# Kernel tuning notes

Hardware: AMD Instinct MI355X
Metric: run time of the kernel (lower is better)

The kernel has to match this reference:

```python
import jax, jax.numpy as jnp
import numpy as np

N, F, H, K = 4096, 512, 256, 8
NEG = -1e9


def _attention(h, mask, a_w, a_b):
    # h: [N,H]; mask: [N,N] bool; a_w: [K,2H]; a_b: [K]
    # per-head logits[i,j] = lrelu(a_src . h_i + a_dst . h_j + b), softmax over
    # neighbors j (A[i,j]==1); out_i = h_i + sum_j alpha_ij h_j; isolated nodes
    # (no neighbors) keep h_i unchanged (alpha row masked to zero).
    Hd = h.shape[1]
    src = h @ a_w[:, :Hd].T + a_b[None, :]   # [N,K]
    dst = h @ a_w[:, Hd:].T                  # [N,K]
    fmask = mask.astype(h.dtype)
    outs = []
    for k in range(a_w.shape[0]):
        logits = jax.nn.leaky_relu(src[:, k][:, None] + dst[:, k][None, :], 0.01)
        logits = jnp.where(mask, logits, NEG)
        alpha = jax.nn.softmax(logits, axis=1) * fmask  # zero rows for isolated nodes
        outs.append(h + alpha @ h)
    return outs


def setup_inputs() -> dict:
    key = jax.random.key(0)
    ks = jax.random.split(key, 12)
    s = 0.02
    adjacency = jax.random.randint(ks[0], (N, N), 0, 2).astype(jnp.float32)
    feats = jax.random.normal(ks[1], (N, F), dtype=jnp.float32)
    return {
        "adjacency": adjacency,
        "feats": feats,
        "W1_w": jax.random.normal(ks[2], (H, F), dtype=jnp.float32) * s,
        "W1_b": jnp.zeros((H,), jnp.float32),
        "a1_w": jax.random.normal(ks[3], (K, 2 * H), dtype=jnp.float32) * s,
        "a1_b": jnp.zeros((K,), jnp.float32),
        "W2_w": jax.random.normal(ks[4], (H, K * H), dtype=jnp.float32) * s,
        "W2_b": jnp.zeros((H,), jnp.float32),
        "a2_w": jax.random.normal(ks[5], (K, 2 * H), dtype=jnp.float32) * s,
        "a2_b": jnp.zeros((K,), jnp.float32),
        "out_w": jax.random.normal(ks[6], (1, H), dtype=jnp.float32) * s,
        "out_b": jnp.zeros((1,), jnp.float32),
    }


def reference(adjacency, feats, W1_w, W1_b, a1_w, a1_b, W2_w, W2_b, a2_w, a2_b, out_w, out_b):
    mask = adjacency == 1.0
    # torch.inner(A, feats.T) == A @ feats; dropout is identity in eval mode
    h1 = (adjacency @ feats) @ W1_w.T + W1_b            # [N,H]
    heads1 = _attention(h1, mask, a1_w, a1_b)           # K x [N,H]
    h1_new = jax.nn.elu(jnp.concatenate(heads1, axis=1))  # [N,K*H]
    h2 = h1_new @ W2_w.T + W2_b                         # [N,H]
    heads2 = _attention(h2, mask, a2_w, a2_b)
    avg = sum(heads2) / a2_w.shape[0]                   # [N,H]
    h2_new = jax.nn.elu(avg)
    avgd = jnp.mean(h2_new, axis=0)                     # [H]
    return avgd @ out_w.T + out_b                       # [1]
```

## Files before the change

### kernel.cpp

```cpp
#include <hip/hip_runtime.h>
#include <hip/hip_bf16.h>
#include <hip/hip_fp16.h>


#define NN 4096
#define FF 512
#define HH 256
#define KK 8
#define KH 2048

typedef __attribute__((ext_vector_type(8))) short bf16x8;
typedef __attribute__((ext_vector_type(4))) float f32x4;
typedef __attribute__((ext_vector_type(16))) float f32x16;
typedef _Float16 h16x2 __attribute__((ext_vector_type(2)));
typedef _Float16 h16x8 __attribute__((ext_vector_type(8)));

__device__ inline short f2bf(float x) {
    __hip_bfloat16 b = __float2bfloat16(x);
    return *reinterpret_cast<short*>(&b);
}
__device__ inline short to_bf(float x) { return f2bf(x); }
__device__ inline short to_bf(short x) { return x; }

__device__ inline unsigned int pkh(float a, float b) {
    auto r = __builtin_amdgcn_cvt_pkrtz(a, b);
    unsigned int u;
    __builtin_memcpy(&u, &r, 4);
    return u;
}
__device__ inline unsigned int h2mul(unsigned int a, unsigned int b) {
    h16x2 av, bv;
    __builtin_memcpy(&av, &a, 4);
    __builtin_memcpy(&bv, &b, 4);
    h16x2 r = av * bv;
    unsigned int u;
    __builtin_memcpy(&u, &r, 4);
    return u;
}
__device__ inline unsigned int h2max(unsigned int a, unsigned int b) {
    h16x2 av, bv;
    __builtin_memcpy(&av, &a, 4);
    __builtin_memcpy(&bv, &b, 4);
    h16x2 r = __builtin_elementwise_max(av, bv);
    unsigned int u;
    __builtin_memcpy(&u, &r, 4);
    return u;
}
__device__ inline float h2dot1(unsigned int a, float c) {
    h16x2 av;
    __builtin_memcpy(&av, &a, 4);
    h16x2 one = {(_Float16)1.0f, (_Float16)1.0f};
    return __builtin_amdgcn_fdot2(av, one, c, false);
}

__device__ inline unsigned int enc_f(float x) {
    unsigned int u = __float_as_uint(x);
    return (u & 0x80000000u) ? ~u : (u | 0x80000000u);
}
__device__ inline float dec_f(unsigned int e) {
    unsigned int u = (e & 0x80000000u) ? (e ^ 0x80000000u) : ~e;
    return __uint_as_float(u);
}

__global__ void pack_mask_kernel(const float* __restrict__ adj,
                                 unsigned int* __restrict__ mbits) {
    int i = blockIdx.x;
    int lane = threadIdx.x & 63;
    int wv = threadIdx.x >> 6;
    for (int j0 = wv * 64; j0 < NN; j0 += 256) {
        float v = adj[(size_t)i * NN + j0 + lane];
        unsigned long long b = __ballot(v == 1.0f);
        if (lane == 0) {
            mbits[i * 128 + (j0 >> 5)]     = (unsigned int)(b & 0xffffffffull);
            mbits[i * 128 + (j0 >> 5) + 1] = (unsigned int)(b >> 32);
        }
    }
}

template <typename T>
__global__ __launch_bounds__(256) void cvt_a_frag_kernel(const T* __restrict__ src,
                                                         bf16x8* __restrict__ dst, int K) {
    int t = threadIdx.x, lane = t & 63, w = t >> 6, mt = blockIdx.x;
    int Kt = K >> 5;
    int m = mt * 16 + (lane & 15), kq = (lane >> 4) * 8;
    for (int kt = w; kt < Kt; kt += 4) {
        size_t base = (size_t)m * K + kt * 32 + kq;
        bf16x8 v;
#pragma unroll
        for (int jj = 0; jj < 8; jj++) v[jj] = to_bf(src[base + jj]);
        dst[((size_t)mt * Kt + kt) * 64 + lane] = v;
    }
}

__global__ __launch_bounds__(256) void cvt_bt_frag_kernel(const float* __restrict__ Wm,
                                                          bf16x8* __restrict__ dst,
                                                          int K, int Nt) {
    int t = threadIdx.x, lane = t & 63, w = t >> 6, nt = blockIdx.x;
    int Kt = K >> 5;
    int n = nt * 16 + (lane & 15), kq = (lane >> 4) * 8;
    for (int kt = w; kt < Kt; kt += 4) {
        size_t base = (size_t)n * K + kt * 32 + kq;
        bf16x8 v;
#pragma unroll
        for (int jj = 0; jj < 8; jj++) v[jj] = f2bf(Wm[base + jj]);
        dst[((size_t)kt * Nt + nt) * 64 + lane] = v;
    }
}

template <int W>
__global__ __launch_bounds__(256) void cvt_b_frag_kernel(const float* __restrict__ src,
                                                         bf16x8* __restrict__ dst) {
    __shared__ float hs[32][W + 8];
    constexpr int Nt = W / 16;
    int t = threadIdx.x, jb = blockIdx.x;
    {
        int r = t >> 3, cb = (t & 7) * (W / 8);
        const float* sp = &src[(size_t)(jb * 32 + r) * W + cb];
#pragma unroll
        for (int q = 0; q < W / 32; q++) *(float4*)&hs[r][cb + q * 4] = *(const float4*)&sp[q * 4];
    }
    __syncthreads();
    for (int id = t; id < Nt * 64; id += 256) {
        int nt = id >> 6, lane = id & 63;
        int c = nt * 16 + (lane & 15), q8 = (lane >> 4) * 8;
        bf16x8 v;
#pragma unroll
        for (int jj = 0; jj < 8; jj++) v[jj] = f2bf(hs[q8 + jj][c]);
        dst[((size_t)jb * Nt + nt) * 64 + lane] = v;
    }
}

__global__ __launch_bounds__(256) void gemm_frag_kernel(
    const bf16x8* __restrict__ Af, const bf16x8* __restrict__ Bf,
    const float* __restrict__ bias, float* __restrict__ C,
    int Kt, int Nt, int Nrow) {
    int t = threadIdx.x, lane = t & 63, w = t >> 6;
    int quad = lane >> 4, c16 = lane & 15;
    int wm = w & 1, wn = w >> 1;
    int mt0 = blockIdx.y * 4 + wm * 2;
    int nt0 = blockIdx.x * 8 + wn * 4;
    f32x4 acc[2][4];
#pragma unroll
    for (int i = 0; i < 2; i++)
#pragma unroll
        for (int j = 0; j < 4; j++) acc[i][j] = (f32x4){0.f, 0.f, 0.f, 0.f};
    const bf16x8* ap = Af + (size_t)mt0 * Kt * 64 + lane;
    const bf16x8* bp = Bf + (size_t)nt0 * 64 + lane;
#pragma unroll 2
    for (int kt = 0; kt < Kt; kt++) {
        bf16x8 a0 = ap[(size_t)kt * 64];
        bf16x8 a1 = ap[((size_t)Kt + kt) * 64];
        bf16x8 b0 = bp[(size_t)kt * Nt * 64];
        bf16x8 b1 = bp[((size_t)kt * Nt + 1) * 64];
        bf16x8 b2 = bp[((size_t)kt * Nt + 2) * 64];
        bf16x8 b3 = bp[((size_t)kt * Nt + 3) * 64];
        acc[0][0] = __builtin_amdgcn_mfma_f32_16x16x32_bf16(a0, b0, acc[0][0], 0, 0, 0);
        acc[0][1] = __builtin_amdgcn_mfma_f32_16x16x32_bf16(a0, b1, acc[0][1], 0, 0, 0);
        acc[0][2] = __builtin_amdgcn_mfma_f32_16x16x32_bf16(a0, b2, acc[0][2], 0, 0, 0);
        acc[0][3] = __builtin_amdgcn_mfma_f32_16x16x32_bf16(a0, b3, acc[0][3], 0, 0, 0);
        acc[1][0] = __builtin_amdgcn_mfma_f32_16x16x32_bf16(a1, b0, acc[1][0], 0, 0, 0);
        acc[1][1] = __builtin_amdgcn_mfma_f32_16x16x32_bf16(a1, b1, acc[1][1], 0, 0, 0);
        acc[1][2] = __builtin_amdgcn_mfma_f32_16x16x32_bf16(a1, b2, acc[1][2], 0, 0, 0);
        acc[1][3] = __builtin_amdgcn_mfma_f32_16x16x32_bf16(a1, b3, acc[1][3], 0, 0, 0);
    }
#pragma unroll
    for (int i = 0; i < 2; i++) {
#pragma unroll
        for (int j = 0; j < 4; j++) {
            int n = (nt0 + j) * 16 + c16;
            float bv = bias ? bias[n] : 0.f;
#pragma unroll
            for (int reg = 0; reg < 4; reg++) {
                int m = (mt0 + i) * 16 + quad * 4 + reg;
                C[(size_t)m * Nrow + n] = acc[i][j][reg] + bv;
            }
        }
    }
}

__global__ __launch_bounds__(256) void gemm_adj_kernel(
    const unsigned int* __restrict__ mbits, const bf16x8* __restrict__ Bf,
    float* __restrict__ C, int Kt, int Nt, int Nrow) {
    int t = threadIdx.x, lane = t & 63, w = t >> 6;
    int quad = lane >> 4, c16 = lane & 15;
    int wm = w & 1, wn = w >> 1;
    int mt0 = blockIdx.y * 4 + wm * 2;
    int nt0 = blockIdx.x * 8 + wn * 4;
    int m = lane & 15, q8 = (lane >> 4) * 8;
    int row0 = mt0 * 16 + m, row1 = row0 + 16;
    f32x4 acc[2][4];
#pragma unroll
    for (int i = 0; i < 2; i++)
#pragma unroll
        for (int j = 0; j < 4; j++) acc[i][j] = (f32x4){0.f, 0.f, 0.f, 0.f};
    const bf16x8* bp = Bf + (size_t)nt0 * 64 + lane;
#pragma unroll 2
    for (int kt = 0; kt < Kt; kt++) {
        unsigned int w0 = mbits[(size_t)row0 * 128 + kt];
        unsigned int w1 = mbits[(size_t)row1 * 128 + kt];
        unsigned int mb0 = (w0 >> q8) & 0xffu;
        unsigned int mb1 = (w1 >> q8) & 0xffu;
        union { unsigned int u[4]; bf16x8 v; } A0, A1;
#pragma unroll
        for (int jp = 0; jp < 4; jp++) {
            unsigned int u0 = (mb0 >> (2 * jp)) & 3u;
            unsigned int u1 = (mb1 >> (2 * jp)) & 3u;
            A0.u[jp] = ((u0 * 0x8001u) & 0x10001u) * 0x3F80u;
            A1.u[jp] = ((u1 * 0x8001u) & 0x10001u) * 0x3F80u;
        }
        bf16x8 b0 = bp[(size_t)kt * Nt * 64];
        bf16x8 b1 = bp[((size_t)kt * Nt + 1) * 64];
        bf16x8 b2 = bp[((size_t)kt * Nt + 2) * 64];
        bf16x8 b3 = bp[((size_t)kt * Nt + 3) * 64];
        acc[0][0] = __builtin_amdgcn_mfma_f32_16x16x32_bf16(A0.v, b0, acc[0][0], 0, 0, 0);
        acc[0][1] = __builtin_amdgcn_mfma_f32_16x16x32_bf16(A0.v, b1, acc[0][1], 0, 0, 0);
        acc[0][2] = __builtin_amdgcn_mfma_f32_16x16x32_bf16(A0.v, b2, acc[0][2], 0, 0, 0);
        acc[0][3] = __builtin_amdgcn_mfma_f32_16x16x32_bf16(A0.v, b3, acc[0][3], 0, 0, 0);
        acc[1][0] = __builtin_amdgcn_mfma_f32_16x16x32_bf16(A1.v, b0, acc[1][0], 0, 0, 0);
        acc[1][1] = __builtin_amdgcn_mfma_f32_16x16x32_bf16(A1.v, b1, acc[1][1], 0, 0, 0);
        acc[1][2] = __builtin_amdgcn_mfma_f32_16x16x32_bf16(A1.v, b2, acc[1][2], 0, 0, 0);
        acc[1][3] = __builtin_amdgcn_mfma_f32_16x16x32_bf16(A1.v, b3, acc[1][3], 0, 0, 0);
    }
#pragma unroll
    for (int i = 0; i < 2; i++) {
#pragma unroll
        for (int j = 0; j < 4; j++) {
            int n = (nt0 + j) * 16 + c16;
#pragma unroll
            for (int reg = 0; reg < 4; reg++) {
                int mm = (mt0 + i) * 16 + quad * 4 + reg;
                C[(size_t)mm * Nrow + n] = acc[i][j][reg];
            }
        }
    }
}

__global__ __launch_bounds__(256) void prep_kernel(const float* __restrict__ h,
                                                   const float* __restrict__ aw,
                                                   const float* __restrict__ ab,
                                                   h16x8* __restrict__ HB16,
                                                   float* __restrict__ srcT,
                                                   float* __restrict__ dstT,
                                                   unsigned int* __restrict__ maxd_u) {
    __shared__ __align__(16) float hs[32][264];
    __shared__ __align__(16) float awl[KK * 512];
    int t = threadIdx.x, jb = blockIdx.x;
#pragma unroll
    for (int q = 0; q < 4; q++)
        *(float4*)&awl[(t + q * 256) * 4] = *(const float4*)&aw[(t + q * 256) * 4];
    {
        int r = t >> 3, cb = (t & 7) * 32;
        const float* hp = &h[(size_t)(jb * 32 + r) * HH + cb];
#pragma unroll
        for (int q = 0; q < 8; q++) *(float4*)&hs[r][cb + q * 4] = *(const float4*)&hp[q * 4];
    }
    __syncthreads();
#pragma unroll
    for (int it = 0; it < 4; it++) {
        int id = t + it * 256;
        int q = id >> 9, nt = (id >> 6) & 7, lane = id & 63;
        int c = nt * 32 + (lane & 31), j8 = q * 16 + (lane >> 5) * 8;
        union { unsigned int u[4]; h16x8 v; } pk;
#pragma unroll
        for (int jp = 0; jp < 4; jp++)
            pk.u[jp] = pkh(hs[j8 + 2 * jp][c], hs[j8 + 2 * jp + 1][c]);
        HB16[((size_t)(jb * 2 + q)) * 512 + nt * 64 + lane] = pk.v;
    }
    {
        const float LOG2E = 1.4426950408889634f;
        int row = t & 31, head = t >> 5;
        float s = ab[head], d = 0.f;
        const float* ws = &awl[head * 512];
        const float* wd = ws + 256;
#pragma unroll 4
        for (int c = 0; c < 256; c += 4) {
            float4 hv = *(const float4*)&hs[row][c];
            float4 a4 = *(const float4*)&ws[c];
            float4 b4 = *(const float4*)&wd[c];
            s += hv.x * a4.x + hv.y * a4.y + hv.z * a4.z + hv.w * a4.w;
            d += hv.x * b4.x + hv.y * b4.y + hv.z * b4.z + hv.w * b4.w;
        }
        float ds = d * LOG2E;
        srcT[head * NN + jb * 32 + row] = s * LOG2E;
        dstT[head * NN + jb * 32 + row] = ds;
        float mx = ds;
#pragma unroll
        for (int off = 16; off > 0; off >>= 1) mx = fmaxf(mx, __shfl_xor(mx, off));
        if (row == 0) atomicMax(&maxd_u[head], enc_f(mx));
    }
}

template <int MODE>
__global__ __launch_bounds__(256, 2) void attn32_kernel(
    const float* __restrict__ h, const float* __restrict__ srcT,
    const float* __restrict__ dstT, const unsigned int* __restrict__ maxd_u,
    const unsigned int* __restrict__ mbits, const h16x8* __restrict__ HB16,
    void* __restrict__ outp) {
    __shared__ __align__(16) char smraw[49600];
    __shared__ float l_all[2][2][32];
    __shared__ float linv_l[2][32];
    unsigned short* e1t = (unsigned short*)smraw;
    unsigned short* e2t = (unsigned short*)(smraw + 16384);
    unsigned int* mrow = (unsigned int*)(smraw + 32768);
    float* accbuf = (float*)smraw;

    int t = threadIdx.x;
    int i0 = blockIdx.x * 32;
    int k0 = blockIdx.y * 2;

    float Dv0 = dec_f(maxd_u[k0]), Dv1 = dec_f(maxd_u[k0 + 1]);
#pragma unroll
    for (int q = 0; q < 8; q++) {
        int idx = t + q * 256;
        int hh = idx >> 10, off = (idx & 1023) * 4;
        float D = hh ? Dv1 : Dv0;
        float4 dv = *(const float4*)&dstT[(size_t)(k0 + hh) * NN + off];
        float d0 = dv.x - D, d1 = dv.y - D, d2 = dv.z - D, d3 = dv.w - D;
        uint2 p1, p2;
        p1.x = pkh(__builtin_amdgcn_exp2f(d0), __builtin_amdgcn_exp2f(d1));
        p1.y = pkh(__builtin_amdgcn_exp2f(d2), __builtin_amdgcn_exp2f(d3));
        p2.x = pkh(__builtin_amdgcn_exp2f(0.01f * d0), __builtin_amdgcn_exp2f(0.01f * d1));
        p2.y = pkh(__builtin_amdgcn_exp2f(0.01f * d2), __builtin_amdgcn_exp2f(0.01f * d3));
        *(uint2*)&e1t[hh * 4096 + off] = p1;
        *(uint2*)&e2t[hh * 4096 + off] = p2;
    }
#pragma unroll
    for (int q = 0; q < 16; q++) {
        int idx = t + q * 256;
        int r = idx >> 7, wd = idx & 127;
        mrow[r * 131 + wd] = mbits[(size_t)(i0 + r) * 128 + wd];
    }
    __syncthreads();

    int lane = t & 63, w = t >> 6;
    int jh = w & 1, ch = w >> 1;
    int rowl = lane & 31, jsub = (lane >> 5) * 8;

    unsigned int AcPk[2], BcPk[2];
    float lacc[2] = {0.f, 0.f};
#pragma unroll
    for (int hh = 0; hh < 2; hh++) {
        float sL = srcT[(size_t)(k0 + hh) * NN + i0 + rowl];
        float xm = sL + (hh ? Dv1 : Dv0);
        float mL = fmaxf(xm, 0.01f * xm);
        float Acf = __builtin_amdgcn_exp2f(xm - mL);
        float Bcf = __builtin_amdgcn_exp2f(fmaf(0.01f, xm, -mL));
        AcPk[hh] = pkh(Acf, Acf);
        BcPk[hh] = pkh(Bcf, Bcf);
    }

    f32x16 acc[2][4];
#pragma unroll
    for (int hh = 0; hh < 2; hh++)
#pragma unroll
        for (int nt = 0; nt < 4; nt++)
#pragma unroll
            for (int r = 0; r < 16; r++) acc[hh][nt][r] = 0.f;

    const unsigned short* e1b0 = e1t;
    const unsigned short* e1b1 = e1t + 4096;
    const unsigned short* e2b0 = e2t;
    const unsigned short* e2b1 = e2t + 4096;

    for (int jj0 = 0; jj0 < 64; jj0++) {
        int jbg = jh * 64 + jj0;
        unsigned int word = mrow[rowl * 131 + jbg];
#pragma unroll
        for (int s = 0; s < 2; s++) {
            int j16 = jbg * 2 + s;
            unsigned int mb = (word >> (s * 16 + jsub)) & 0xffu;
            unsigned int mw[4];
#pragma unroll
            for (int jp = 0; jp < 4; jp++) {
                unsigned int u2 = (mb >> (2 * jp)) & 3u;
                mw[jp] = ((u2 * 0x8001u) & 0x10001u) * 0xffffu;
            }
            int eoff = j16 * 16 + jsub;
            union { unsigned int u[4]; h16x8 v; } P[2];
            {
                uint4 E1 = *(const uint4*)&e1b0[eoff];
                uint4 E2 = *(const uint4*)&e2b0[eoff];
                unsigned int v0 = h2max(h2mul(E1.x, AcPk[0]), h2mul(E2.x, BcPk[0])) & mw[0];
                unsigned int v1 = h2max(h2mul(E1.y, AcPk[0]), h2mul(E2.y, BcPk[0])) & mw[1];
                unsigned int v2 = h2max(h2mul(E1.z, AcPk[0]), h2mul(E2.z, BcPk[0])) & mw[2];
                unsigned int v3 = h2max(h2mul(E1.w, AcPk[0]), h2mul(E2.w, BcPk[0])) & mw[3];
                lacc[0] = h2dot1(v0, lacc[0]);
                lacc[0] = h2dot1(v1, lacc[0]);
                lacc[0] = h2dot1(v2, lacc[0]);
                lacc[0] = h2dot1(v3, lacc[0]);
                P[0].u[0] = v0; P[0].u[1] = v1; P[0].u[2] = v2; P[0].u[3] = v3;
            }
            {
                uint4 E1 = *(const uint4*)&e1b1[eoff];
                uint4 E2 = *(const uint4*)&e2b1[eoff];
                unsigned int v0 = h2max(h2mul(E1.x, AcPk[1]), h2mul(E2.x, BcPk[1])) & mw[0];
                unsigned int v1 = h2max(h2mul(E1.y, AcPk[1]), h2mul(E2.y, BcPk[1])) & mw[1];
                unsigned int v2 = h2max(h2mul(E1.z, AcPk[1]), h2mul(E2.z, BcPk[1])) & mw[2];
                unsigned int v3 = h2max(h2mul(E1.w, AcPk[1]), h2mul(E2.w, BcPk[1])) & mw[3];
                lacc[1] = h2dot1(v0, lacc[1]);
                lacc[1] = h2dot1(v1, lacc[1]);
                lacc[1] = h2dot1(v2, lacc[1]);
                lacc[1] = h2dot1(v3, lacc[1]);
                P[1].u[0] = v0; P[1].u[1] = v1; P[1].u[2] = v2; P[1].u[3] = v3;
            }
            const h16x8* bp = &HB16[(size_t)j16 * 512 + (ch * 4) * 64 + lane];
#pragma unroll
            for (int nt = 0; nt < 4; nt++) {
                h16x8 bv = bp[nt * 64];
                acc[0][nt] = __builtin_amdgcn_mfma_f32_32x32x16_f16(P[0].v, bv, acc[0][nt], 0, 0, 0);
                acc[1][nt] = __builtin_amdgcn_mfma_f32_32x32x16_f16(P[1].v, bv, acc[1][nt], 0, 0, 0);
            }
        }
    }

    lacc[0] += __shfl_xor(lacc[0], 32);
    lacc[1] += __shfl_xor(lacc[1], 32);
    if (ch == 0 && lane < 32) {
        l_all[jh][0][lane] = lacc[0];
        l_all[jh][1][lane] = lacc[1];
    }
    __syncthreads();
    if (t < 32) {
#pragma unroll
        for (int hh = 0; hh < 2; hh++) {
            float lt = l_all[0][hh][t] + l_all[1][hh][t];
            linv_l[hh][t] = (lt > 0.f) ? 1.f / lt : 0.f;
        }
    }
    __syncthreads();

#pragma unroll
    for (int r = 0; r < 2; r++) {
        if (jh == 1) {
#pragma unroll
            for (int nt = 0; nt < 4; nt++) {
                float* dp = accbuf + (size_t)((ch * 4 + nt) * 16) * 64 + lane;
#pragma unroll
                for (int reg = 0; reg < 16; reg++) dp[reg * 64] = acc[r][nt][reg];
            }
        }
        __syncthreads();
        if (jh == 0) {
            int khead = k0 + r;
#pragma unroll
            for (int nt = 0; nt < 4; nt++) {
                const float* sp = accbuf + (size_t)((ch * 4 + nt) * 16) * 64 + lane;
                int c = (ch * 4 + nt) * 32 + (lane & 31);
#pragma unroll
                for (int reg = 0; reg < 16; reg++) {
                    int rowloc = (reg & 3) + 8 * (reg >> 2) + 4 * (lane >> 5);
                    float v = (acc[r][nt][reg] + sp[reg * 64]) * linv_l[r][rowloc];
                    int i = i0 + rowloc;
                    if (MODE == 1) {
                        v += h[(size_t)i * HH + c];
                        v = (v > 0.f) ? v : (__expf(v) - 1.f);
                        ((short*)outp)[(size_t)i * KH + (size_t)khead * HH + c] = f2bf(v);
                    } else {
                        ((short*)outp)[(size_t)khead * NN * HH + (size_t)i * HH + c] = f2bf(v);
                    }
                }
            }
        }
        if (r == 0) __syncthreads();
    }
}

__global__ void colsum_kernel(const float* __restrict__ h2,
                              const short* __restrict__ heads,
                              float* __restrict__ partial) {
    int c = threadIdx.x;
    int b = blockIdx.x;
    float s = 0.f;
    for (int il = 0; il < 64; il++) {
        int i = b * 64 + il;
        float v = h2[(size_t)i * HH + c];
#pragma unroll
        for (int k = 0; k < KK; k++) {
            unsigned int bits = (unsigned int)(unsigned short)heads[(size_t)k * NN * HH + (size_t)i * HH + c];
            v += 0.125f * __uint_as_float(bits << 16);
        }
        s += (v > 0.f) ? v : (__expf(v) - 1.f);
    }
    partial[b * HH + c] = s;
}

__global__ void final_kernel(const float* __restrict__ partial,
                             const float* __restrict__ out_w,
                             const float* __restrict__ out_b,
                             float* __restrict__ dout) {
    __shared__ float red[256];
    int c = threadIdx.x;
    float s = 0.f;
    for (int b = 0; b < 64; b++) s += partial[b * HH + c];
    red[c] = (s / 4096.f) * out_w[c];
    __syncthreads();
    for (int off = 128; off > 0; off >>= 1) {
        if (c < off) red[c] += red[c + off];
        __syncthreads();
    }
    if (c == 0) dout[0] = red[0] + out_b[0];
}

extern "C" void kernel_launch(void* const* d_in, const int* in_sizes, int n_in,
                              void* d_out, int out_size, void* d_ws, size_t ws_size,
                              hipStream_t stream) {
    (void)in_sizes; (void)n_in; (void)out_size; (void)ws_size;
    const float* adj   = (const float*)d_in[0];
    const float* feats = (const float*)d_in[1];
    const float* W1_w  = (const float*)d_in[2];
    const float* W1_b  = (const float*)d_in[3];
    const float* a1_w  = (const float*)d_in[4];
    const float* a1_b  = (const float*)d_in[5];
    const float* W2_w  = (const float*)d_in[6];
    const float* W2_b  = (const float*)d_in[7];
    const float* a2_w  = (const float*)d_in[8];
    const float* a2_b  = (const float*)d_in[9];
    const float* out_w = (const float*)d_in[10];
    const float* out_b = (const float*)d_in[11];

    char* w = (char*)d_ws;
    const size_t MB = 1ull << 20;
    unsigned int* mbits = (unsigned int*)(w);
    short*  h1nb   = (short*)(w + 2 * MB);
    bf16x8* h1na   = (bf16x8*)(w + 18 * MB);
    short*  planes = (short*)(w + 2 * MB);
    bf16x8* Bfeats = (bf16x8*)(w + 34 * MB);
    float*  h2     = (float*)(w + 34 * MB);
    float*  tmp1   = (float*)(w + 38 * MB);
    float*  h1     = (float*)(w + 38 * MB);
    bf16x8* W1f    = (bf16x8*)(w + 42 * MB);
    bf16x8* W2f    = (bf16x8*)(w + 42 * MB + 256 * 1024);
    float*  srcT   = (float*)(w + 43 * MB + 256 * 1024);
    float*  dstT   = (float*)(w + 43 * MB + 384 * 1024);
    unsigned int* maxd_u = (unsigned int*)(w + 43 * MB + 512 * 1024);
    h16x8*  HB16   = (h16x8*)(w + 44 * MB);
    bf16x8* tmp1a  = (bf16x8*)(w + 46 * MB);
    float*  partial = (float*)(w + 50 * MB);

    pack_mask_kernel<<<NN, 256, 0, stream>>>(adj, mbits);
    cvt_b_frag_kernel<FF><<<NN / 32, 256, 0, stream>>>(feats, Bfeats);
    gemm_adj_kernel<<<dim3(FF / 128, NN / 64), 256, 0, stream>>>(
        mbits, Bfeats, tmp1, NN / 32, FF / 16, FF);
    cvt_a_frag_kernel<float><<<NN / 16, 256, 0, stream>>>(tmp1, tmp1a, FF);
    cvt_bt_frag_kernel<<<HH / 16, 256, 0, stream>>>(W1_w, W1f, FF, HH / 16);
    gemm_frag_kernel<<<dim3(HH / 128, NN / 64), 256, 0, stream>>>(
        tmp1a, W1f, W1_b, h1, FF / 32, HH / 16, HH);

    (void)hipMemsetAsync(maxd_u, 0, KK * sizeof(unsigned int), stream);
    prep_kernel<<<NN / 32, 256, 0, stream>>>(h1, a1_w, a1_b, HB16, srcT, dstT, maxd_u);
    attn32_kernel<1><<<dim3(NN / 32, KK / 2), 256, 0, stream>>>(
        h1, srcT, dstT, maxd_u, mbits, HB16, h1nb);
    cvt_a_frag_kernel<short><<<NN / 16, 256, 0, stream>>>(h1nb, h1na, KH);
    cvt_bt_frag_kernel<<<HH / 16, 256, 0, stream>>>(W2_w, W2f, KH, HH / 16);
    gemm_frag_kernel<<<dim3(HH / 128, NN / 64), 256, 0, stream>>>(
        h1na, W2f, W2_b, h2, KH / 32, HH / 16, HH);

    (void)hipMemsetAsync(maxd_u, 0, KK * sizeof(unsigned int), stream);
    prep_kernel<<<NN / 32, 256, 0, stream>>>(h2, a2_w, a2_b, HB16, srcT, dstT, maxd_u);
    attn32_kernel<2><<<dim3(NN / 32, KK / 2), 256, 0, stream>>>(
        h2, srcT, dstT, maxd_u, mbits, HB16, planes);
    colsum_kernel<<<64, 256, 0, stream>>>(h2, planes, partial);
    final_kernel<<<1, 256, 0, stream>>>(partial, out_w, out_b, (float*)d_out);
}
```

Measured before the change: 462.8 us.

## Shrink GEMM tiles for more blocks, merge weight conversions, interleave attention MFMAs

Both the W1 and W2 weight-fragment conversions now run in one launch, and the workspace is rearranged to fit. gemm_frag and gemm_adj get smaller per-wave tiles and twice as many blocks, which raises occupancy on the many-CU GPU but lowers operand reuse. In the attention kernel, the B fragments are loaded before the P computation and each head's MFMAs are issued as soon as its P is ready. colsum now uses 256 blocks instead of 64, with final_kernel summing more partials to match.

```diff
diff --git a/kernel.cpp b/kernel.cpp
--- a/kernel.cpp
+++ b/kernel.cpp
@@ -92,9 +92,14 @@
     }
 }
 
-__global__ __launch_bounds__(256) void cvt_bt_frag_kernel(const float* __restrict__ Wm,
-                                                          bf16x8* __restrict__ dst,
-                                                          int K, int Nt) {
+__global__ __launch_bounds__(256) void cvt_bt2_kernel(const float* __restrict__ W1,
+                                                      const float* __restrict__ W2,
+                                                      bf16x8* __restrict__ d1,
+                                                      bf16x8* __restrict__ d2) {
+    const float* Wm = blockIdx.y ? W2 : W1;
+    bf16x8* dst = blockIdx.y ? d2 : d1;
+    int K = blockIdx.y ? KH : FF;
+    constexpr int Nt = HH / 16;
     int t = threadIdx.x, lane = t & 63, w = t >> 6, nt = blockIdx.x;
     int Kt = K >> 5;
     int n = nt * 16 + (lane & 15), kq = (lane >> 4) * 8;
@@ -138,35 +143,29 @@
     int quad = lane >> 4, c16 = lane & 15;
     int wm = w & 1, wn = w >> 1;
     int mt0 = blockIdx.y * 4 + wm * 2;
-    int nt0 = blockIdx.x * 8 + wn * 4;
-    f32x4 acc[2][4];
+    int nt0 = blockIdx.x * 4 + wn * 2;
+    f32x4 acc[2][2];
 #pragma unroll
     for (int i = 0; i < 2; i++)
 #pragma unroll
-        for (int j = 0; j < 4; j++) acc[i][j] = (f32x4){0.f, 0.f, 0.f, 0.f};
+        for (int j = 0; j < 2; j++) acc[i][j] = (f32x4){0.f, 0.f, 0.f, 0.f};
     const bf16x8* ap = Af + (size_t)mt0 * Kt * 64 + lane;
     const bf16x8* bp = Bf + (size_t)nt0 * 64 + lane;
-#pragma unroll 2
+#pragma unroll 4
     for (int kt = 0; kt < Kt; kt++) {
         bf16x8 a0 = ap[(size_t)kt * 64];
         bf16x8 a1 = ap[((size_t)Kt + kt) * 64];
         bf16x8 b0 = bp[(size_t)kt * Nt * 64];
         bf16x8 b1 = bp[((size_t)kt * Nt + 1) * 64];
-        bf16x8 b2 = bp[((size_t)kt * Nt + 2) * 64];
-        bf16x8 b3 = bp[((size_t)kt * Nt + 3) * 64];
         acc[0][0] = __builtin_amdgcn_mfma_f32_16x16x32_bf16(a0, b0, acc[0][0], 0, 0, 0);
         acc[0][1] = __builtin_amdgcn_mfma_f32_16x16x32_bf16(a0, b1, acc[0][1], 0, 0, 0);
-        acc[0][2] = __builtin_amdgcn_mfma_f32_16x16x32_bf16(a0, b2, acc[0][2], 0, 0, 0);
-        acc[0][3] = __builtin_amdgcn_mfma_f32_16x16x32_bf16(a0, b3, acc[0][3], 0, 0, 0);
         acc[1][0] = __builtin_amdgcn_mfma_f32_16x16x32_bf16(a1, b0, acc[1][0], 0, 0, 0);
         acc[1][1] = __builtin_amdgcn_mfma_f32_16x16x32_bf16(a1, b1, acc[1][1], 0, 0, 0);
-        acc[1][2] = __builtin_amdgcn_mfma_f32_16x16x32_bf16(a1, b2, acc[1][2], 0, 0, 0);
-        acc[1][3] = __builtin_amdgcn_mfma_f32_16x16x32_bf16(a1, b3, acc[1][3], 0, 0, 0);
     }
 #pragma unroll
     for (int i = 0; i < 2; i++) {
 #pragma unroll
-        for (int j = 0; j < 4; j++) {
+        for (int j = 0; j < 2; j++) {
             int n = (nt0 + j) * 16 + c16;
             float bv = bias ? bias[n] : 0.f;
 #pragma unroll
@@ -184,53 +183,39 @@
     int t = threadIdx.x, lane = t & 63, w = t >> 6;
     int quad = lane >> 4, c16 = lane & 15;
     int wm = w & 1, wn = w >> 1;
-    int mt0 = blockIdx.y * 4 + wm * 2;
+    int mt = blockIdx.y * 2 + wm;
     int nt0 = blockIdx.x * 8 + wn * 4;
-    int m = lane & 15, q8 = (lane >> 4) * 8;
-    int row0 = mt0 * 16 + m, row1 = row0 + 16;
-    f32x4 acc[2][4];
-#pragma unroll
-    for (int i = 0; i < 2; i++)
-#pragma unroll
-        for (int j = 0; j < 4; j++) acc[i][j] = (f32x4){0.f, 0.f, 0.f, 0.f};
+    int row = mt * 16 + (lane & 15), q8 = (lane >> 4) * 8;
+    f32x4 acc[4];
+#pragma unroll
+    for (int j = 0; j < 4; j++) acc[j] = (f32x4){0.f, 0.f, 0.f, 0.f};
     const bf16x8* bp = Bf + (size_t)nt0 * 64 + lane;
 #pragma unroll 2
     for (int kt = 0; kt < Kt; kt++) {
-        unsigned int w0 = mbits[(size_t)row0 * 128 + kt];
-        unsigned int w1 = mbits[(size_t)row1 * 128 + kt];
+        unsigned int w0 = mbits[(size_t)row * 128 + kt];
         unsigned int mb0 = (w0 >> q8) & 0xffu;
-        unsigned int mb1 = (w1 >> q8) & 0xffu;
-        union { unsigned int u[4]; bf16x8 v; } A0, A1;
+        union { unsigned int u[4]; bf16x8 v; } A0;
 #pragma unroll
         for (int jp = 0; jp < 4; jp++) {
             unsigned int u0 = (mb0 >> (2 * jp)) & 3u;
-            unsigned int u1 = (mb1 >> (2 * jp)) & 3u;
             A0.u[jp] = ((u0 * 0x8001u) & 0x10001u) * 0x3F80u;
-            A1.u[jp] = ((u1 * 0x8001u) & 0x10001u) * 0x3F80u;
         }
         bf16x8 b0 = bp[(size_t)kt * Nt * 64];
         bf16x8 b1 = bp[((size_t)kt * Nt + 1) * 64];
         bf16x8 b2 = bp[((size_t)kt * Nt + 2) * 64];
         bf16x8 b3 = bp[((size_t)kt * Nt + 3) * 64];
-        acc[0][0] = __builtin_amdgcn_mfma_f32_16x16x32_bf16(A0.v, b0, acc[0][0], 0, 0, 0);
-        acc[0][1] = __builtin_amdgcn_mfma_f32_16x16x32_bf16(A0.v, b1, acc[0][1], 0, 0, 0);
-        acc[0][2] = __builtin_amdgcn_mfma_f32_16x16x32_bf16(A0.v, b2, acc[0][2], 0, 0, 0);
-        acc[0][3] = __builtin_amdgcn_mfma_f32_16x16x32_bf16(A0.v, b3, acc[0][3], 0, 0, 0);
-        acc[1][0] = __builtin_amdgcn_mfma_f32_16x16x32_bf16(A1.v, b0, acc[1][0], 0, 0, 0);
-        acc[1][1] = __builtin_amdgcn_mfma_f32_16x16x32_bf16(A1.v, b1, acc[1][1], 0, 0, 0);
-        acc[1][2] = __builtin_amdgcn_mfma_f32_16x16x32_bf16(A1.v, b2, acc[1][2], 0, 0, 0);
-        acc[1][3] = __builtin_amdgcn_mfma_f32_16x16x32_bf16(A1.v, b3, acc[1][3], 0, 0, 0);
-    }
-#pragma unroll
-    for (int i = 0; i < 2; i++) {
-#pragma unroll
-        for (int j = 0; j < 4; j++) {
-            int n = (nt0 + j) * 16 + c16;
-#pragma unroll
-            for (int reg = 0; reg < 4; reg++) {
-                int mm = (mt0 + i) * 16 + quad * 4 + reg;
-                C[(size_t)mm * Nrow + n] = acc[i][j][reg];
-            }
+        acc[0] = __builtin_amdgcn_mfma_f32_16x16x32_bf16(A0.v, b0, acc[0], 0, 0, 0);
+        acc[1] = __builtin_amdgcn_mfma_f32_16x16x32_bf16(A0.v, b1, acc[1], 0, 0, 0);
+        acc[2] = __builtin_amdgcn_mfma_f32_16x16x32_bf16(A0.v, b2, acc[2], 0, 0, 0);
+        acc[3] = __builtin_amdgcn_mfma_f32_16x16x32_bf16(A0.v, b3, acc[3], 0, 0, 0);
+    }
+#pragma unroll
+    for (int j = 0; j < 4; j++) {
+        int n = (nt0 + j) * 16 + c16;
+#pragma unroll
+        for (int reg = 0; reg < 4; reg++) {
+            int mm = mt * 16 + quad * 4 + reg;
+            C[(size_t)mm * Nrow + n] = acc[j][reg];
         }
     }
 }
@@ -376,7 +361,9 @@
                 mw[jp] = ((u2 * 0x8001u) & 0x10001u) * 0xffffu;
             }
             int eoff = j16 * 16 + jsub;
-            union { unsigned int u[4]; h16x8 v; } P[2];
+            const h16x8* bp = &HB16[(size_t)j16 * 512 + (ch * 4) * 64 + lane];
+            h16x8 bv0 = bp[0], bv1 = bp[64], bv2 = bp[128], bv3 = bp[192];
+            union { unsigned int u[4]; h16x8 v; } P0;
             {
                 uint4 E1 = *(const uint4*)&e1b0[eoff];
                 uint4 E2 = *(const uint4*)&e2b0[eoff];
@@ -388,8 +375,13 @@
                 lacc[0] = h2dot1(v1, lacc[0]);
                 lacc[0] = h2dot1(v2, lacc[0]);
                 lacc[0] = h2dot1(v3, lacc[0]);
-                P[0].u[0] = v0; P[0].u[1] = v1; P[0].u[2] = v2; P[0].u[3] = v3;
+                P0.u[0] = v0; P0.u[1] = v1; P0.u[2] = v2; P0.u[3] = v3;
             }
+            acc[0][0] = __builtin_amdgcn_mfma_f32_32x32x16_f16(P0.v, bv0, acc[0][0], 0, 0, 0);
+            acc[0][1] = __builtin_amdgcn_mfma_f32_32x32x16_f16(P0.v, bv1, acc[0][1], 0, 0, 0);
+            acc[0][2] = __builtin_amdgcn_mfma_f32_32x32x16_f16(P0.v, bv2, acc[0][2], 0, 0, 0);
+            acc[0][3] = __builtin_amdgcn_mfma_f32_32x32x16_f16(P0.v, bv3, acc[0][3], 0, 0, 0);
+            union { unsigned int u[4]; h16x8 v; } P1;
             {
                 uint4 E1 = *(const uint4*)&e1b1[eoff];
                 uint4 E2 = *(const uint4*)&e2b1[eoff];
@@ -401,15 +393,12 @@
                 lacc[1] = h2dot1(v1, lacc[1]);
                 lacc[1] = h2dot1(v2, lacc[1]);
                 lacc[1] = h2dot1(v3, lacc[1]);
-                P[1].u[0] = v0; P[1].u[1] = v1; P[1].u[2] = v2; P[1].u[3] = v3;
+                P1.u[0] = v0; P1.u[1] = v1; P1.u[2] = v2; P1.u[3] = v3;
             }
-            const h16x8* bp = &HB16[(size_t)j16 * 512 + (ch * 4) * 64 + lane];
-#pragma unroll
-            for (int nt = 0; nt < 4; nt++) {
-                h16x8 bv = bp[nt * 64];
-                acc[0][nt] = __builtin_amdgcn_mfma_f32_32x32x16_f16(P[0].v, bv, acc[0][nt], 0, 0, 0);
-                acc[1][nt] = __builtin_amdgcn_mfma_f32_32x32x16_f16(P[1].v, bv, acc[1][nt], 0, 0, 0);
-            }
+            acc[1][0] = __builtin_amdgcn_mfma_f32_32x32x16_f16(P1.v, bv0, acc[1][0], 0, 0, 0);
+            acc[1][1] = __builtin_amdgcn_mfma_f32_32x32x16_f16(P1.v, bv1, acc[1][1], 0, 0, 0);
+            acc[1][2] = __builtin_amdgcn_mfma_f32_32x32x16_f16(P1.v, bv2, acc[1][2], 0, 0, 0);
+            acc[1][3] = __builtin_amdgcn_mfma_f32_32x32x16_f16(P1.v, bv3, acc[1][3], 0, 0, 0);
         }
     }
 
@@ -471,8 +460,8 @@
     int c = threadIdx.x;
     int b = blockIdx.x;
     float s = 0.f;
-    for (int il = 0; il < 64; il++) {
-        int i = b * 64 + il;
+    for (int il = 0; il < 16; il++) {
+        int i = b * 16 + il;
         float v = h2[(size_t)i * HH + c];
 #pragma unroll
         for (int k = 0; k < KK; k++) {
@@ -491,7 +480,7 @@
     __shared__ float red[256];
     int c = threadIdx.x;
     float s = 0.f;
-    for (int b = 0; b < 64; b++) s += partial[b * HH + c];
+    for (int b = 0; b < 256; b++) s += partial[b * HH + c];
     red[c] = (s / 4096.f) * out_w[c];
     __syncthreads();
     for (int off = 128; off > 0; off >>= 1) {
@@ -520,30 +509,31 @@
 
     char* w = (char*)d_ws;
     const size_t MB = 1ull << 20;
+    const size_t KB = 1ull << 10;
     unsigned int* mbits = (unsigned int*)(w);
+    bf16x8* Bfeats = (bf16x8*)(w + 2 * MB);
+    float*  tmp1   = (float*)(w + 6 * MB);
+    bf16x8* tmp1a  = (bf16x8*)(w + 14 * MB);
     short*  h1nb   = (short*)(w + 2 * MB);
+    short*  planes = (short*)(w + 2 * MB);
     bf16x8* h1na   = (bf16x8*)(w + 18 * MB);
-    short*  planes = (short*)(w + 2 * MB);
-    bf16x8* Bfeats = (bf16x8*)(w + 34 * MB);
     float*  h2     = (float*)(w + 34 * MB);
-    float*  tmp1   = (float*)(w + 38 * MB);
     float*  h1     = (float*)(w + 38 * MB);
-    bf16x8* W1f    = (bf16x8*)(w + 42 * MB);
-    bf16x8* W2f    = (bf16x8*)(w + 42 * MB + 256 * 1024);
-    float*  srcT   = (float*)(w + 43 * MB + 256 * 1024);
-    float*  dstT   = (float*)(w + 43 * MB + 384 * 1024);
-    unsigned int* maxd_u = (unsigned int*)(w + 43 * MB + 512 * 1024);
-    h16x8*  HB16   = (h16x8*)(w + 44 * MB);
-    bf16x8* tmp1a  = (bf16x8*)(w + 46 * MB);
-    float*  partial = (float*)(w + 50 * MB);
+    h16x8*  HB16   = (h16x8*)(w + 42 * MB);
+    bf16x8* W1f    = (bf16x8*)(w + 44 * MB);
+    bf16x8* W2f    = (bf16x8*)(w + 44 * MB + 256 * KB);
+    float*  srcT   = (float*)(w + 45 * MB + 256 * KB);
+    float*  dstT   = (float*)(w + 45 * MB + 384 * KB);
+    unsigned int* maxd_u = (unsigned int*)(w + 45 * MB + 512 * KB);
+    float*  partial = (float*)(w + 45 * MB + 768 * KB);
 
     pack_mask_kernel<<<NN, 256, 0, stream>>>(adj, mbits);
     cvt_b_frag_kernel<FF><<<NN / 32, 256, 0, stream>>>(feats, Bfeats);
-    gemm_adj_kernel<<<dim3(FF / 128, NN / 64), 256, 0, stream>>>(
+    cvt_bt2_kernel<<<dim3(HH / 16, 2), 256, 0, stream>>>(W1_w, W2_w, W1f, W2f);
+    gemm_adj_kernel<<<dim3(FF / 128, NN / 32), 256, 0, stream>>>(
         mbits, Bfeats, tmp1, NN / 32, FF / 16, FF);
     cvt_a_frag_kernel<float><<<NN / 16, 256, 0, stream>>>(tmp1, tmp1a, FF);
-    cvt_bt_frag_kernel<<<HH / 16, 256, 0, stream>>>(W1_w, W1f, FF, HH / 16);
-    gemm_frag_kernel<<<dim3(HH / 128, NN / 64), 256, 0, stream>>>(
+    gemm_frag_kernel<<<dim3(HH / 64, NN / 64), 256, 0, stream>>>(
         tmp1a, W1f, W1_b, h1, FF / 32, HH / 16, HH);
 
     (void)hipMemsetAsync(maxd_u, 0, KK * sizeof(unsigned int), stream);
@@ -551,14 +541,13 @@
     attn32_kernel<1><<<dim3(NN / 32, KK / 2), 256, 0, stream>>>(
         h1, srcT, dstT, maxd_u, mbits, HB16, h1nb);
     cvt_a_frag_kernel<short><<<NN / 16, 256, 0, stream>>>(h1nb, h1na, KH);
-    cvt_bt_frag_kernel<<<HH / 16, 256, 0, stream>>>(W2_w, W2f, KH, HH / 16);
-    gemm_frag_kernel<<<dim3(HH / 128, NN / 64), 256, 0, stream>>>(
+    gemm_frag_kernel<<<dim3(HH / 64, NN / 64), 256, 0, stream>>>(
         h1na, W2f, W2_b, h2, KH / 32, HH / 16, HH);
 
     (void)hipMemsetAsync(maxd_u, 0, KK * sizeof(unsigned int), stream);
     prep_kernel<<<NN / 32, 256, 0, stream>>>(h2, a2_w, a2_b, HB16, srcT, dstT, maxd_u);
     attn32_kernel<2><<<dim3(NN / 32, KK / 2), 256, 0, stream>>>(
         h2, srcT, dstT, maxd_u, mbits, HB16, planes);
-    colsum_kernel<<<64, 256, 0, stream>>>(h2, planes, partial);
+    colsum_kernel<<<256, 256, 0, stream>>>(h2, planes, partial);
     final_kernel<<<1, 256, 0, stream>>>(partial, out_w, out_b, (float*)d_out);
 }
```

Measured after the change: 450.5 us. 2.7% less time.
